# Kernel tuning notes

Measured on AMD Instinct MI355X. Metric: run time of the kernel, lower is better.

The kernel has to match this reference:

```python
import jax, jax.numpy as jnp
import numpy as np

B, D, H, O, A = 16384, 128, 128, 32, 64  # batch, state_dim, num_neurons, num_options, num_actions


def setup_inputs() -> dict:
    key = jax.random.key(0)
    ks = jax.random.split(key, 16)
    s = 0.05
    return {
        "state": jax.random.normal(ks[0], (B, D), dtype=jnp.float32),
        "u": jax.random.uniform(ks[1], (B,), dtype=jnp.float32),
        # option network: Linear(D,H) -> ReLU -> Linear(H,O)
        "opt_w1": jax.random.normal(ks[2], (D, H), dtype=jnp.float32) * s,
        "opt_b1": jnp.zeros((H,), dtype=jnp.float32),
        "opt_w2": jax.random.normal(ks[3], (H, O), dtype=jnp.float32) * s,
        "opt_b2": jnp.zeros((O,), dtype=jnp.float32),
        # per-option expert MLPs (num_layers=1): Linear(D,H) -> ReLU -> Linear(H,A)
        "exp_w1": jax.random.normal(ks[4], (O, D, H), dtype=jnp.float32) * s,
        "exp_b1": jnp.zeros((O, H), dtype=jnp.float32),
        "exp_w2": jax.random.normal(ks[5], (O, H, A), dtype=jnp.float32) * s,
        "exp_b2": jnp.zeros((O, A), dtype=jnp.float32),
        # termination network: Linear(D,H) -> ReLU -> Linear(H,1) -> Sigmoid
        "term_w1": jax.random.normal(ks[6], (D, H), dtype=jnp.float32) * s,
        "term_b1": jnp.zeros((H,), dtype=jnp.float32),
        "term_w2": jax.random.normal(ks[7], (H, 1), dtype=jnp.float32) * s,
        "term_b2": jnp.zeros((1,), dtype=jnp.float32),
    }


def reference(state, u, opt_w1, opt_b1, opt_w2, opt_b2,
              exp_w1, exp_b1, exp_w2, exp_b2,
              term_w1, term_b1, term_w2, term_b2):
    num_options = opt_w2.shape[-1]
    # option head
    opt_h = jax.nn.relu(state @ opt_w1 + opt_b1)
    option_probs = jax.nn.softmax(opt_h @ opt_w2 + opt_b2, axis=-1)  # [B,O]
    # multinomial(option_probs, 1) via inverse-CDF with provided uniforms u
    cdf = jnp.cumsum(option_probs, axis=-1)
    selected_options = jnp.minimum((cdf < u[:, None]).sum(-1), num_options - 1).astype(jnp.int32)  # [B]
    selected_options = jax.lax.stop_gradient(selected_options)
    # routed per-sample expert MLP (gather weights, batched matmuls)
    w1 = exp_w1[selected_options]  # [B,D,H]
    b1 = exp_b1[selected_options]  # [B,H]
    h = jax.nn.relu(jnp.einsum('bd,bdh->bh', state, w1) + b1)
    logits = jnp.einsum('bh,bha->ba', h, exp_w2[selected_options]) + exp_b2[selected_options]
    action_probs = jax.nn.softmax(logits, axis=-1)  # [B,A]
    selected_actions = jnp.argmax(action_probs, axis=-1)  # [B]
    # termination head
    term_h = jax.nn.relu(state @ term_w1 + term_b1)
    termination_prob = jax.nn.sigmoid(term_h @ term_w2 + term_b2)  # [B,1]
    return option_probs, action_probs, termination_prob, selected_options, selected_actions
```

## Files before the change

kernel.cpp:

```cpp
#include <hip/hip_runtime.h>
#include <math.h>

constexpr int B = 16384;
constexpr int D = 128;
constexpr int H = 128;
constexpr int O = 32;
constexpr int A = 64;

constexpr int NB1 = 32;
constexpr int NT1 = 256;
constexpr int NBLK1 = B / NB1;
constexpr int TS    = 32;
constexpr int NT2   = 256;
constexpr int SLOTS = 32;


__global__ __launch_bounds__(NT1) void phase1(
    const float* __restrict__ state, const float* __restrict__ u,
    const float* __restrict__ opt_w1, const float* __restrict__ opt_b1,
    const float* __restrict__ opt_w2, const float* __restrict__ opt_b2,
    const float* __restrict__ term_w1, const float* __restrict__ term_b1,
    const float* __restrict__ term_w2, const float* __restrict__ term_b2,
    float* __restrict__ out_optp, float* __restrict__ out_term,
    float* __restrict__ out_selopt, int* __restrict__ ws_sel)
{
    __shared__ float s_x[NB1][D];
    __shared__ float s_probs[NB1][O];
    __shared__ float s_term[NB1];

    const int tid   = threadIdx.x;
    const bool isOpt = blockIdx.x < (unsigned)NBLK1;
    const int b0    = (blockIdx.x & (NBLK1 - 1)) * NB1;

    #pragma unroll
    for (int i = 0; i < 4; ++i) {
        const int lin = tid + i * NT1;
        const int row = lin >> 5, col = (lin & 31) << 2;
        *(float4*)&s_x[row][col] =
            *(const float4*)&state[(size_t)(b0 + row) * D + col];
    }
    __syncthreads();

    const int q  = tid & 31;
    const int n4 = q << 2;
    const int g  = tid >> 5;
    const int s0 = g << 2;

    if (isOpt) {
        float4 accO[4];
        {
            const float4 bO = *(const float4*)&opt_b1[n4];
            #pragma unroll
            for (int j = 0; j < 4; ++j) accO[j] = bO;
        }
        #pragma unroll 4
        for (int d = 0; d < D; d += 4) {
            float4 wO[4];
            #pragma unroll
            for (int i = 0; i < 4; ++i)
                wO[i] = *(const float4*)&opt_w1[(d + i) * H + n4];
            #pragma unroll
            for (int j = 0; j < 4; ++j) {
                const float4 x = *(const float4*)&s_x[s0 + j][d];
                const float xs[4] = {x.x, x.y, x.z, x.w};
                #pragma unroll
                for (int i = 0; i < 4; ++i) {
                    accO[j].x = fmaf(xs[i], wO[i].x, accO[j].x);
                    accO[j].y = fmaf(xs[i], wO[i].y, accO[j].y);
                    accO[j].z = fmaf(xs[i], wO[i].z, accO[j].z);
                    accO[j].w = fmaf(xs[i], wO[i].w, accO[j].w);
                }
            }
        }
        __syncthreads();
        #pragma unroll
        for (int j = 0; j < 4; ++j) {
            float4 h;
            h.x = fmaxf(accO[j].x, 0.f); h.y = fmaxf(accO[j].y, 0.f);
            h.z = fmaxf(accO[j].z, 0.f); h.w = fmaxf(accO[j].w, 0.f);
            *(float4*)&s_x[s0 + j][n4] = h;
        }
        __syncthreads();

        {
            const int o  = tid & 31;
            const int t0 = (tid >> 5) << 2;
            float acc4[4];
            {
                const float bb = opt_b2[o];
                #pragma unroll
                for (int j = 0; j < 4; ++j) acc4[j] = bb;
            }
            for (int h = 0; h < H; h += 4) {
                const float w0 = opt_w2[(h + 0) * O + o];
                const float w1 = opt_w2[(h + 1) * O + o];
                const float w2 = opt_w2[(h + 2) * O + o];
                const float w3 = opt_w2[(h + 3) * O + o];
                #pragma unroll
                for (int j = 0; j < 4; ++j) {
                    const float4 hv = *(const float4*)&s_x[t0 + j][h];
                    acc4[j] = fmaf(hv.x, w0, acc4[j]);
                    acc4[j] = fmaf(hv.y, w1, acc4[j]);
                    acc4[j] = fmaf(hv.z, w2, acc4[j]);
                    acc4[j] = fmaf(hv.w, w3, acc4[j]);
                }
            }
            #pragma unroll
            for (int j = 0; j < 4; ++j) {
                const float v = acc4[j];
                float m = v;
                #pragma unroll
                for (int mask = 16; mask; mask >>= 1)
                    m = fmaxf(m, __shfl_xor(m, mask, 32));
                const float e = expf(v - m);
                float ss = e;
                #pragma unroll
                for (int mask = 16; mask; mask >>= 1)
                    ss += __shfl_xor(ss, mask, 32);
                const float p = e / ss;
                s_probs[t0 + j][o] = p;
                out_optp[(size_t)(b0 + t0 + j) * O + o] = p;
            }
        }
        __syncthreads();

        if (tid < NB1) {
            const float uu = u[b0 + tid];
            float c = 0.f; int cnt = 0;
            for (int o = 0; o < O; ++o) {
                c += s_probs[tid][o];
                cnt += (c < uu) ? 1 : 0;
            }
            const int sel = (cnt < O - 1) ? cnt : (O - 1);
            out_selopt[b0 + tid] = (float)sel;
            ws_sel[b0 + tid] = sel;
        }
    } else {
        float4 accT[4];
        {
            const float4 bT = *(const float4*)&term_b1[n4];
            #pragma unroll
            for (int j = 0; j < 4; ++j) accT[j] = bT;
        }
        #pragma unroll 4
        for (int d = 0; d < D; d += 4) {
            float4 wT[4];
            #pragma unroll
            for (int i = 0; i < 4; ++i)
                wT[i] = *(const float4*)&term_w1[(d + i) * H + n4];
            #pragma unroll
            for (int j = 0; j < 4; ++j) {
                const float4 x = *(const float4*)&s_x[s0 + j][d];
                const float xs[4] = {x.x, x.y, x.z, x.w};
                #pragma unroll
                for (int i = 0; i < 4; ++i) {
                    accT[j].x = fmaf(xs[i], wT[i].x, accT[j].x);
                    accT[j].y = fmaf(xs[i], wT[i].y, accT[j].y);
                    accT[j].z = fmaf(xs[i], wT[i].z, accT[j].z);
                    accT[j].w = fmaf(xs[i], wT[i].w, accT[j].w);
                }
            }
        }
        const float4 w2v = *(const float4*)&term_w2[n4];
        #pragma unroll
        for (int j = 0; j < 4; ++j) {
            float t = fmaxf(accT[j].x, 0.f) * w2v.x + fmaxf(accT[j].y, 0.f) * w2v.y
                    + fmaxf(accT[j].z, 0.f) * w2v.z + fmaxf(accT[j].w, 0.f) * w2v.w;
            #pragma unroll
            for (int mask = 16; mask; mask >>= 1)
                t += __shfl_xor(t, mask, 32);
            if (q == 0) s_term[s0 + j] = t;
        }
        __syncthreads();
        if (tid < NB1) {
            const float x = s_term[tid] + term_b2[0];
            out_term[b0 + tid] = 1.f / (1.f + expf(-x));
        }
    }
}

__global__ __launch_bounds__(256) void mid(
    const int* __restrict__ ws_sel, unsigned short* __restrict__ bucket,
    int* __restrict__ counts, int* __restrict__ offsets)
{
    __shared__ int s_wsum[4];
    __shared__ int s_lt4[4];
    const int o    = blockIdx.x;
    const int tid  = threadIdx.x;
    const int lane = tid & 63, wv = tid >> 6;
    const int4* sp = (const int4*)ws_sel + tid * 16;

    int ce = 0, cl = 0;
    #pragma unroll 4
    for (int k = 0; k < 16; ++k) {
        const int4 v = sp[k];
        ce += (v.x == o) + (v.y == o) + (v.z == o) + (v.w == o);
        cl += (v.x <  o) + (v.y <  o) + (v.z <  o) + (v.w <  o);
    }
    int inc = ce;
    #pragma unroll
    for (int offd = 1; offd < 64; offd <<= 1) {
        const int t2 = __shfl_up(inc, offd, 64);
        if (lane >= offd) inc += t2;
    }
    int lt = cl;
    #pragma unroll
    for (int mask = 32; mask; mask >>= 1) lt += __shfl_xor(lt, mask, 64);
    if (lane == 63) s_wsum[wv] = inc;
    if (lane == 0)  s_lt4[wv]  = lt;
    __syncthreads();
    int wbase = 0;
    for (int w = 0; w < wv; ++w) wbase += s_wsum[w];
    const int ltotal = s_lt4[0] + s_lt4[1] + s_lt4[2] + s_lt4[3];
    int pos = ltotal + wbase + inc - ce;

    #pragma unroll 4
    for (int k = 0; k < 16; ++k) {
        const int4 v = sp[k];
        const int i0 = (tid * 16 + k) * 4;
        if (v.x == o) bucket[pos++] = (unsigned short)(i0);
        if (v.y == o) bucket[pos++] = (unsigned short)(i0 + 1);
        if (v.z == o) bucket[pos++] = (unsigned short)(i0 + 2);
        if (v.w == o) bucket[pos++] = (unsigned short)(i0 + 3);
    }
    if (tid == 255) {
        counts[o]  = wbase + inc;
        offsets[o] = ltotal;
    }
}

__global__ __launch_bounds__(NT2) void phase2(
    const float* __restrict__ state,
    const float* __restrict__ exp_w1, const float* __restrict__ exp_b1,
    const float* __restrict__ exp_w2, const float* __restrict__ exp_b2,
    float* __restrict__ out_actp, float* __restrict__ out_selact,
    const int* __restrict__ counts, const int* __restrict__ offsets,
    const unsigned short* __restrict__ bucket)
{
    __shared__ float s_x2[TS][D + 4];
    __shared__ int   s_idx[TS];

    const int slot = blockIdx.x;
    const int o    = blockIdx.y;
    const int cnt  = counts[o];
    const int off  = offsets[o];
    const int tid  = threadIdx.x;
    const float* w1p = exp_w1 + (size_t)o * D * H;
    const float* w2p = exp_w2 + (size_t)o * H * A;

    const int q  = tid & 31, n4 = q << 2;
    const int g2 = tid >> 5, s02 = g2 << 2;
    const int a4 = (tid & 15) << 2, tg = tid >> 4;

    for (int t = slot; t * TS < cnt; t += SLOTS) {
        const int start = t * TS;
        const int nloc  = min(TS, cnt - start);

        __syncthreads();
        if (tid < TS) s_idx[tid] = (tid < nloc) ? (int)bucket[off + start + tid] : 0;
        __syncthreads();

        #pragma unroll
        for (int i = 0; i < 4; ++i) {
            const int lin = tid + i * NT2;
            const int row = lin >> 5, col = (lin & 31) << 2;
            float4 v = make_float4(0.f, 0.f, 0.f, 0.f);
            if (row < nloc)
                v = *(const float4*)&state[(size_t)s_idx[row] * D + col];
            *(float4*)&s_x2[row][col] = v;
        }
        __syncthreads();

        float4 acc[4];
        {
            const float4 bia = *(const float4*)&exp_b1[o * H + n4];
            #pragma unroll
            for (int j = 0; j < 4; ++j) acc[j] = bia;
        }
        #pragma unroll 4
        for (int d = 0; d < D; d += 4) {
            float4 w[4];
            #pragma unroll
            for (int i = 0; i < 4; ++i)
                w[i] = *(const float4*)&w1p[(d + i) * H + n4];
            #pragma unroll
            for (int j = 0; j < 4; ++j) {
                const float4 x = *(const float4*)&s_x2[s02 + j][d];
                const float xs[4] = {x.x, x.y, x.z, x.w};
                #pragma unroll
                for (int i = 0; i < 4; ++i) {
                    acc[j].x = fmaf(xs[i], w[i].x, acc[j].x);
                    acc[j].y = fmaf(xs[i], w[i].y, acc[j].y);
                    acc[j].z = fmaf(xs[i], w[i].z, acc[j].z);
                    acc[j].w = fmaf(xs[i], w[i].w, acc[j].w);
                }
            }
        }
        __syncthreads();
        #pragma unroll
        for (int j = 0; j < 4; ++j) {
            float4 h;
            h.x = fmaxf(acc[j].x, 0.f); h.y = fmaxf(acc[j].y, 0.f);
            h.z = fmaxf(acc[j].z, 0.f); h.w = fmaxf(acc[j].w, 0.f);
            *(float4*)&s_x2[s02 + j][n4] = h;
        }
        __syncthreads();

        float4 la[2];
        la[0] = make_float4(0.f, 0.f, 0.f, 0.f);
        la[1] = la[0];
        #pragma unroll 4
        for (int h = 0; h < H; h += 4) {
            float4 w[4];
            #pragma unroll
            for (int i = 0; i < 4; ++i)
                w[i] = *(const float4*)&w2p[(h + i) * A + a4];
            #pragma unroll
            for (int j = 0; j < 2; ++j) {
                const float4 x = *(const float4*)&s_x2[tg * 2 + j][h];
                const float xs[4] = {x.x, x.y, x.z, x.w};
                #pragma unroll
                for (int i = 0; i < 4; ++i) {
                    la[j].x = fmaf(xs[i], w[i].x, la[j].x);
                    la[j].y = fmaf(xs[i], w[i].y, la[j].y);
                    la[j].z = fmaf(xs[i], w[i].z, la[j].z);
                    la[j].w = fmaf(xs[i], w[i].w, la[j].w);
                }
            }
        }
        const float4 bias2 = *(const float4*)&exp_b2[o * A + a4];

        #pragma unroll
        for (int j = 0; j < 2; ++j) {
            const int srow = tg * 2 + j;
            float4 v;
            v.x = la[j].x + bias2.x; v.y = la[j].y + bias2.y;
            v.z = la[j].z + bias2.z; v.w = la[j].w + bias2.w;
            float m = fmaxf(fmaxf(v.x, v.y), fmaxf(v.z, v.w));
            #pragma unroll
            for (int mask = 8; mask; mask >>= 1)
                m = fmaxf(m, __shfl_xor(m, mask, 16));
            float4 e;
            e.x = expf(v.x - m); e.y = expf(v.y - m);
            e.z = expf(v.z - m); e.w = expf(v.w - m);
            float ss = e.x + e.y + e.z + e.w;
            #pragma unroll
            for (int mask = 8; mask; mask >>= 1)
                ss += __shfl_xor(ss, mask, 16);
            const float inv = 1.f / ss;
            float4 p;
            p.x = e.x * inv; p.y = e.y * inv; p.z = e.z * inv; p.w = e.w * inv;
            float bv = p.x; int bi = a4;
            if (p.y > bv) { bv = p.y; bi = a4 + 1; }
            if (p.z > bv) { bv = p.z; bi = a4 + 2; }
            if (p.w > bv) { bv = p.w; bi = a4 + 3; }
            #pragma unroll
            for (int mask = 8; mask; mask >>= 1) {
                const float ov = __shfl_xor(bv, mask, 16);
                const int   oi = __shfl_xor(bi, mask, 16);
                if (ov > bv || (ov == bv && oi < bi)) { bv = ov; bi = oi; }
            }
            if (srow < nloc) {
                const int gidx = s_idx[srow];
                *(float4*)&out_actp[(size_t)gidx * A + a4] = p;
                if ((tid & 15) == 0) out_selact[gidx] = (float)bi;
            }
        }
    }
}

extern "C" void kernel_launch(void* const* d_in, const int* in_sizes, int n_in,
                              void* d_out, int out_size, void* d_ws, size_t ws_size,
                              hipStream_t stream) {
    const float* state   = (const float*)d_in[0];
    const float* u       = (const float*)d_in[1];
    const float* opt_w1  = (const float*)d_in[2];
    const float* opt_b1  = (const float*)d_in[3];
    const float* opt_w2  = (const float*)d_in[4];
    const float* opt_b2  = (const float*)d_in[5];
    const float* exp_w1  = (const float*)d_in[6];
    const float* exp_b1  = (const float*)d_in[7];
    const float* exp_w2  = (const float*)d_in[8];
    const float* exp_b2  = (const float*)d_in[9];
    const float* term_w1 = (const float*)d_in[10];
    const float* term_b1 = (const float*)d_in[11];
    const float* term_w2 = (const float*)d_in[12];
    const float* term_b2 = (const float*)d_in[13];

    float* out = (float*)d_out;
    float* out_optp   = out;
    float* out_actp   = out_optp + (size_t)B * O;
    float* out_term   = out_actp + (size_t)B * A;
    float* out_selopt = out_term + B;
    float* out_selact = out_selopt + B;

    int* wsi = (int*)d_ws;
    int* ws_sel = wsi;
    unsigned short* bucket = (unsigned short*)(wsi + B);
    int* counts  = wsi + B + B / 2;
    int* offsets = counts + 32;

    hipLaunchKernelGGL(phase1, dim3(2 * NBLK1), dim3(NT1), 0, stream,
                       state, u, opt_w1, opt_b1, opt_w2, opt_b2,
                       term_w1, term_b1, term_w2, term_b2,
                       out_optp, out_term, out_selopt, ws_sel);
    hipLaunchKernelGGL(mid, dim3(O), dim3(256), 0, stream,
                       ws_sel, bucket, counts, offsets);
    hipLaunchKernelGGL(phase2, dim3(SLOTS, O), dim3(NT2), 0, stream,
                       state, exp_w1, exp_b1, exp_w2, exp_b2,
                       out_actp, out_selact, counts, offsets, bucket);
}
```

Baseline: 152.3 us.

## Bucket samples by option with atomics in phase1 and drop mid kernel

Phase1 now appends each sample index into a per-option bucket using a global atomicAdd on a counter, instead of writing a selection array that a separate counting/prefix-scan kernel turns into buckets. This removes one kernel launch and its pass over the selections, but adds a memset launch and contended atomics on 32 counters. Bucket order within an option is no longer deterministic, and the buckets grow to a fixed O*B int layout. The unroll factor of phase2's first matmul loop is also raised from 4 to 8.

```diff
diff --git a/kernel.cpp b/kernel.cpp
--- a/kernel.cpp
+++ b/kernel.cpp
@@ -22,7 +22,8 @@
     const float* __restrict__ term_w1, const float* __restrict__ term_b1,
     const float* __restrict__ term_w2, const float* __restrict__ term_b2,
     float* __restrict__ out_optp, float* __restrict__ out_term,
-    float* __restrict__ out_selopt, int* __restrict__ ws_sel)
+    float* __restrict__ out_selopt,
+    int* __restrict__ counts, int* __restrict__ bucket)
 {
     __shared__ float s_x[NB1][D];
     __shared__ float s_probs[NB1][O];
@@ -133,7 +134,8 @@
             }
             const int sel = (cnt < O - 1) ? cnt : (O - 1);
             out_selopt[b0 + tid] = (float)sel;
-            ws_sel[b0 + tid] = sel;
+            const int pos = atomicAdd(&counts[sel], 1);
+            bucket[sel * B + pos] = b0 + tid;
         }
     } else {
         float4 accT[4];
@@ -179,63 +181,12 @@
     }
 }
 
-__global__ __launch_bounds__(256) void mid(
-    const int* __restrict__ ws_sel, unsigned short* __restrict__ bucket,
-    int* __restrict__ counts, int* __restrict__ offsets)
-{
-    __shared__ int s_wsum[4];
-    __shared__ int s_lt4[4];
-    const int o    = blockIdx.x;
-    const int tid  = threadIdx.x;
-    const int lane = tid & 63, wv = tid >> 6;
-    const int4* sp = (const int4*)ws_sel + tid * 16;
-
-    int ce = 0, cl = 0;
-    #pragma unroll 4
-    for (int k = 0; k < 16; ++k) {
-        const int4 v = sp[k];
-        ce += (v.x == o) + (v.y == o) + (v.z == o) + (v.w == o);
-        cl += (v.x <  o) + (v.y <  o) + (v.z <  o) + (v.w <  o);
-    }
-    int inc = ce;
-    #pragma unroll
-    for (int offd = 1; offd < 64; offd <<= 1) {
-        const int t2 = __shfl_up(inc, offd, 64);
-        if (lane >= offd) inc += t2;
-    }
-    int lt = cl;
-    #pragma unroll
-    for (int mask = 32; mask; mask >>= 1) lt += __shfl_xor(lt, mask, 64);
-    if (lane == 63) s_wsum[wv] = inc;
-    if (lane == 0)  s_lt4[wv]  = lt;
-    __syncthreads();
-    int wbase = 0;
-    for (int w = 0; w < wv; ++w) wbase += s_wsum[w];
-    const int ltotal = s_lt4[0] + s_lt4[1] + s_lt4[2] + s_lt4[3];
-    int pos = ltotal + wbase + inc - ce;
-
-    #pragma unroll 4
-    for (int k = 0; k < 16; ++k) {
-        const int4 v = sp[k];
-        const int i0 = (tid * 16 + k) * 4;
-        if (v.x == o) bucket[pos++] = (unsigned short)(i0);
-        if (v.y == o) bucket[pos++] = (unsigned short)(i0 + 1);
-        if (v.z == o) bucket[pos++] = (unsigned short)(i0 + 2);
-        if (v.w == o) bucket[pos++] = (unsigned short)(i0 + 3);
-    }
-    if (tid == 255) {
-        counts[o]  = wbase + inc;
-        offsets[o] = ltotal;
-    }
-}
-
 __global__ __launch_bounds__(NT2) void phase2(
     const float* __restrict__ state,
     const float* __restrict__ exp_w1, const float* __restrict__ exp_b1,
     const float* __restrict__ exp_w2, const float* __restrict__ exp_b2,
     float* __restrict__ out_actp, float* __restrict__ out_selact,
-    const int* __restrict__ counts, const int* __restrict__ offsets,
-    const unsigned short* __restrict__ bucket)
+    const int* __restrict__ counts, const int* __restrict__ bucket)
 {
     __shared__ float s_x2[TS][D + 4];
     __shared__ int   s_idx[TS];
@@ -243,7 +194,7 @@
     const int slot = blockIdx.x;
     const int o    = blockIdx.y;
     const int cnt  = counts[o];
-    const int off  = offsets[o];
+    const int off  = o * B;
     const int tid  = threadIdx.x;
     const float* w1p = exp_w1 + (size_t)o * D * H;
     const float* w2p = exp_w2 + (size_t)o * H * A;
@@ -257,7 +208,7 @@
         const int nloc  = min(TS, cnt - start);
 
         __syncthreads();
-        if (tid < TS) s_idx[tid] = (tid < nloc) ? (int)bucket[off + start + tid] : 0;
+        if (tid < TS) s_idx[tid] = (tid < nloc) ? bucket[off + start + tid] : 0;
         __syncthreads();
 
         #pragma unroll
@@ -277,7 +228,7 @@
             #pragma unroll
             for (int j = 0; j < 4; ++j) acc[j] = bia;
         }
-        #pragma unroll 4
+        #pragma unroll 8
         for (int d = 0; d < D; d += 4) {
             float4 w[4];
             #pragma unroll
@@ -394,19 +345,16 @@
     float* out_selopt = out_term + B;
     float* out_selact = out_selopt + B;
 
-    int* wsi = (int*)d_ws;
-    int* ws_sel = wsi;
-    unsigned short* bucket = (unsigned short*)(wsi + B);
-    int* counts  = wsi + B + B / 2;
-    int* offsets = counts + 32;
-
+    int* wsi    = (int*)d_ws;
+    int* counts = wsi;
+    int* bucket = wsi + 32;
+
+    hipMemsetAsync(counts, 0, O * sizeof(int), stream);
     hipLaunchKernelGGL(phase1, dim3(2 * NBLK1), dim3(NT1), 0, stream,
                        state, u, opt_w1, opt_b1, opt_w2, opt_b2,
                        term_w1, term_b1, term_w2, term_b2,
-                       out_optp, out_term, out_selopt, ws_sel);
-    hipLaunchKernelGGL(mid, dim3(O), dim3(256), 0, stream,
-                       ws_sel, bucket, counts, offsets);
+                       out_optp, out_term, out_selopt, counts, bucket);
     hipLaunchKernelGGL(phase2, dim3(SLOTS, O), dim3(NT2), 0, stream,
                        state, exp_w1, exp_b1, exp_w2, exp_b2,
-                       out_actp, out_selact, counts, offsets, bucket);
+                       out_actp, out_selact, counts, bucket);
 }
```

Result: slower. 175.4 us (+15.1%).
